# Kernel tuning notes

Measured on AMD Instinct MI355X. Metric: run time of the kernel, lower is better.

## Reference

```python
import jax, jax.numpy as jnp
import numpy as np

B, L, H, N, NL = 32, 512, 768, 64, 4
GAIN = 1.0


def layer_norm(x, w, b, eps=1e-5):
    mu = jnp.mean(x, axis=-1, keepdims=True)
    var = jnp.mean((x - mu) ** 2, axis=-1, keepdims=True)
    return (x - mu) * jax.lax.rsqrt(var + eps) * w + b


def setup_inputs() -> dict:
    key = jax.random.key(0)
    ks = jax.random.split(key, 10)
    x = jax.random.normal(ks[0], (B, L, H), dtype=jnp.float32)
    mask = jnp.ones((B, L), dtype=jnp.int32)
    # S4D parameters per layer (stacked over NL)
    log_dt = jnp.log(10.0 ** jax.random.uniform(ks[1], (NL, H), minval=-3.0, maxval=-1.0))
    A_re = jnp.zeros((NL, H, N), dtype=jnp.float32)  # real part = -exp(0) = -1
    A_im = jnp.broadcast_to(np.pi * jnp.arange(N, dtype=jnp.float32), (NL, H, N)).copy()
    C_re = jax.random.normal(ks[2], (NL, 2, H, N), dtype=jnp.float32) * 0.5 ** 0.5
    C_im = jax.random.normal(ks[3], (NL, 2, H, N), dtype=jnp.float32) * 0.5 ** 0.5
    D = jax.random.normal(ks[4], (NL, H), dtype=jnp.float32)
    Wout = jax.random.normal(ks[5], (NL, H, H), dtype=jnp.float32) / np.sqrt(H)
    bout = jnp.zeros((NL, H), dtype=jnp.float32)
    ln1_w = jnp.ones((NL, H), dtype=jnp.float32)
    ln1_b = jnp.zeros((NL, H), dtype=jnp.float32)
    ln2_w = jnp.ones((NL, H), dtype=jnp.float32)
    ln2_b = jnp.zeros((NL, H), dtype=jnp.float32)
    return dict(x=x, mask=mask, ln1_w=ln1_w, ln1_b=ln1_b, log_dt=log_dt,
                A_re=A_re, A_im=A_im, C_re=C_re, C_im=C_im, D=D,
                Wout=Wout, bout=bout, ln2_w=ln2_w, ln2_b=ln2_b)


def bis4(u, mask_f, log_dt, A_re, A_im, C_re, C_im, D, Wout, bout):
    # u: [B, L, H] (post ln_1); mask_f: [B, L] float
    u = (u * mask_f[:, :, None]).transpose(0, 2, 1)  # [B, H, L]
    dt = jnp.exp(log_dt)  # [H]
    A = (-jnp.exp(A_re) + 1j * A_im).astype(jnp.complex64)  # [H, N]
    dtA = dt[:, None] * A  # [H, N]
    C = (C_re + 1j * C_im).astype(jnp.complex64)  # [2, H, N]
    # ZOH-style: K[d,h,l] = 2 Re sum_n C (e^{dtA}-1)/A * e^{dtA l}
    Cw = C * ((jnp.exp(dtA) - 1.0) / A)  # [2, H, N]
    V = jnp.exp(dtA[:, :, None] * jnp.arange(L, dtype=jnp.float32))  # [H, N, L]
    K = 2.0 * jnp.real(jnp.einsum('dhn,hnl->dhl', Cw, V))  # [2, H, L]
    # bidirectional kernel over circular length 2L
    k_full = (jnp.pad(K[0], ((0, 0), (0, L))) +
              jnp.pad(K[1, :, ::-1], ((0, 0), (L, 0))))  # [H, 2L]
    kf = jnp.fft.rfft(k_full, n=2 * L)           # [H, L+1]
    uf = jnp.fft.rfft(u, n=2 * L)                # [B, H, L+1]
    y = jnp.fft.irfft(uf * kf, n=2 * L)[..., :L]  # [B, H, L]
    y = y + D[:, None] * u
    y = jax.nn.gelu(y)
    y = y.transpose(0, 2, 1)  # [B, L, H]
    return jnp.einsum('blh,oh->blo', y, Wout) + bout


def reference(x, mask, ln1_w, ln1_b, log_dt, A_re, A_im, C_re, C_im, D, Wout, bout, ln2_w, ln2_b):
    mask_f = mask.astype(x.dtype)
    for i in range(NL):
        y = layer_norm(x, ln1_w[i], ln1_b[i])
        y = bis4(y, mask_f, log_dt[i], A_re[i], A_im[i], C_re[i], C_im[i], D[i], Wout[i], bout[i])
        y = layer_norm(y, ln2_w[i], ln2_b[i])
        x = x + y * GAIN
    return x
```

## Files before the change

### kernel.cpp

```cpp
#include <hip/hip_runtime.h>
#include <math.h>

#define BB 32
#define LL 512
#define HH 768
#define NN 64
#define NLAYERS 4

typedef unsigned short ushort;
typedef __attribute__((ext_vector_type(8))) short bf16x8;
typedef __attribute__((ext_vector_type(4))) float f32x4;
typedef __attribute__((ext_vector_type(4))) ushort u16x4;

static __device__ __forceinline__ ushort f2bf(float f) {
  union { float f; unsigned u; } v; v.f = f;
  unsigned r = (v.u + 0x7FFF + ((v.u >> 16) & 1)) >> 16;
  return (ushort)r;
}
static __device__ __forceinline__ float bf2f(ushort u) {
  union { unsigned u; float f; } v; v.u = ((unsigned)u) << 16; return v.f;
}
static __device__ __forceinline__ void gload16(const void* g, void* l) {
  __builtin_amdgcn_global_load_lds(
      (const __attribute__((address_space(1))) unsigned int*)g,
      (__attribute__((address_space(3))) unsigned int*)l, 16, 0, 0);
}
static __device__ __forceinline__ float hw_sin(float f) {
#if __has_builtin(__builtin_amdgcn_sinf)
  return __builtin_amdgcn_sinf(f);
#else
  float r; asm("v_sin_f32 %0, %1" : "=v"(r) : "v"(f)); return r;
#endif
}
static __device__ __forceinline__ float hw_cos(float f) {
#if __has_builtin(__builtin_amdgcn_cosf)
  return __builtin_amdgcn_cosf(f);
#else
  float r; asm("v_cos_f32 %0, %1" : "=v"(r) : "v"(f)); return r;
#endif
}

__global__ __launch_bounds__(256) void compute_k_kernel(
    const float* __restrict__ log_dt, const float* __restrict__ A_re,
    const float* __restrict__ A_im, const float* __restrict__ C_re,
    const float* __restrict__ C_im, ushort* __restrict__ rev) {
  __shared__ float4 cons[4][64][5];
  int wid = threadIdx.x >> 6, lane = threadIdx.x & 63;
  int blk = blockIdx.x * 4 + wid;
  int il = blk / HH, h = blk - il * HH;
  {
    int n = lane;
    float dt = expf(log_dt[blk]);
    float a_re = -expf(A_re[(size_t)blk * NN + n]);
    float a_im = A_im[(size_t)blk * NN + n];
    float er = dt * a_re, ei = dt * a_im;
    float ea = __builtin_amdgcn_exp2f(er * 1.4426950408889634f);
    float fr = ei * 0.15915494309189535f;
    fr = fr - floorf(fr);
    float sv = hw_sin(fr), cv = hw_cos(fr);
    float qr = ea * cv, qi = ea * sv;
    float e1r = qr - 1.f, e1i = qi;
    float den = a_re * a_re + a_im * a_im;
    float wr = (e1r * a_re + e1i * a_im) / den;
    float wi = (e1i * a_re - e1r * a_im) / den;
    size_t c0 = ((size_t)(il * 2 + 0) * HH + h) * NN + n;
    size_t c1 = ((size_t)(il * 2 + 1) * HH + h) * NN + n;
    float c0r = C_re[c0], c0i = C_im[c0];
    float c1r = C_re[c1], c1i = C_im[c1];
    float c0wr = 2.f * (c0r * wr - c0i * wi), c0wi = 2.f * (c0r * wi + c0i * wr);
    float c1wr = 2.f * (c1r * wr - c1i * wi), c1wi = 2.f * (c1r * wi + c1i * wr);
    float pr = qr, pi = qi;
    float P[6][2];
#pragma unroll
    for (int j = 0; j < 8; ++j) {
      float nr = pr * pr - pi * pi, ni = 2.f * pr * pi;
      pr = nr; pi = ni;
      if (j >= 2) { P[j - 2][0] = pr; P[j - 2][1] = pi; }
    }
    cons[wid][n][0] = make_float4(qr, qi, c0wr, c0wi);
    cons[wid][n][1] = make_float4(c1wr, c1wi, P[0][0], P[0][1]);
    cons[wid][n][2] = make_float4(P[1][0], P[1][1], P[2][0], P[2][1]);
    cons[wid][n][3] = make_float4(P[3][0], P[3][1], P[4][0], P[4][1]);
    cons[wid][n][4] = make_float4(P[5][0], P[5][1], 0.f, 0.f);
  }
  __syncthreads();
  int t = lane;
  float k0[8], k1[8];
#pragma unroll
  for (int s = 0; s < 8; ++s) { k0[s] = 0.f; k1[s] = 0.f; }
  for (int n = 0; n < NN; ++n) {
    float4 A0 = cons[wid][n][0];
    float4 A1 = cons[wid][n][1];
    float4 A2 = cons[wid][n][2];
    float4 A3 = cons[wid][n][3];
    float4 A4 = cons[wid][n][4];
    float vr = 1.f, vi = 0.f;
#define MULIF(BIT, PR, PI) { bool c = (t & (BIT)) != 0;                       \
    float nr = vr * (PR) - vi * (PI), ni = vr * (PI) + vi * (PR);             \
    vr = c ? nr : vr; vi = c ? ni : vi; }
    MULIF(1,  A1.z, A1.w)
    MULIF(2,  A2.x, A2.y)
    MULIF(4,  A2.z, A2.w)
    MULIF(8,  A3.x, A3.y)
    MULIF(16, A3.z, A3.w)
    MULIF(32, A4.x, A4.y)
#undef MULIF
#pragma unroll
    for (int s = 0; s < 8; ++s) {
      k0[s] = fmaf(A0.z, vr, fmaf(-A0.w, vi, k0[s]));
      k1[s] = fmaf(A1.x, vr, fmaf(-A1.y, vi, k1[s]));
      float nr = vr * A0.x - vi * A0.y;
      float ni = vr * A0.y + vi * A0.x;
      vr = nr; vi = ni;
    }
  }
  ushort* row = rev + ((size_t)blk << 10);
  bf16x8 o0, o1;
#pragma unroll
  for (int i = 0; i < 8; ++i) {
    o0[i] = (short)f2bf(k0[7 - i]);
    o1[i] = (short)f2bf(k1[i]);
  }
  *(bf16x8*)(row + 504 - 8 * t) = o0;
  *(bf16x8*)(row + 512 + 8 * t) = o1;
}

__global__ __launch_bounds__(256) void wcast_kernel(
    const float* __restrict__ W, ushort* __restrict__ Wbf) {
  size_t i = ((size_t)blockIdx.x * 256 + threadIdx.x) * 8;
  float4 a = *(const float4*)&W[i];
  float4 c = *(const float4*)&W[i + 4];
  ushort o[8] = {f2bf(a.x), f2bf(a.y), f2bf(a.z), f2bf(a.w),
                 f2bf(c.x), f2bf(c.y), f2bf(c.z), f2bf(c.w)};
  *(bf16x8*)&Wbf[i] = *(bf16x8*)o;
}

__global__ __launch_bounds__(256) void ln_t_kernel(
    const float* __restrict__ X, const float* __restrict__ w,
    const float* __restrict__ b, const int* __restrict__ mask,
    ushort* __restrict__ U) {
  __shared__ ushort tile[32][772];
  int bb = blockIdx.y;
  int l0 = blockIdx.x << 5;
  int wv = threadIdx.x >> 6, lane = threadIdx.x & 63;
  const float4* w4 = (const float4*)w;
  const float4* b4 = (const float4*)b;
  float4 WW[3], BV[3];
#pragma unroll
  for (int m = 0; m < 3; ++m) { WW[m] = w4[lane + 64 * m]; BV[m] = b4[lane + 64 * m]; }
#pragma unroll
  for (int i = 0; i < 8; ++i) {
    int r = (wv << 3) + i;
    size_t rowi = (size_t)bb * LL + l0 + r;
    const float4* xr = (const float4*)(X + rowi * HH);
    float4 v[3];
    float s = 0.f, s2 = 0.f;
#pragma unroll
    for (int m = 0; m < 3; ++m) {
      v[m] = xr[lane + 64 * m];
      s  += v[m].x + v[m].y + v[m].z + v[m].w;
      s2 += v[m].x * v[m].x + v[m].y * v[m].y + v[m].z * v[m].z + v[m].w * v[m].w;
    }
#pragma unroll
    for (int off = 32; off >= 1; off >>= 1) {
      s  += __shfl_xor(s, off);
      s2 += __shfl_xor(s2, off);
    }
    float mu  = s * (1.f / HH);
    float var = s2 * (1.f / HH) - mu * mu;
    float rs  = rsqrtf(var + 1e-5f);
    float mf  = (float)mask[rowi];
#pragma unroll
    for (int m = 0; m < 3; ++m) {
      u16x4 o;
      o.x = f2bf(((v[m].x - mu) * rs * WW[m].x + BV[m].x) * mf);
      o.y = f2bf(((v[m].y - mu) * rs * WW[m].y + BV[m].y) * mf);
      o.z = f2bf(((v[m].z - mu) * rs * WW[m].z + BV[m].z) * mf);
      o.w = f2bf(((v[m].w - mu) * rs * WW[m].w + BV[m].w) * mf);
      *(u16x4*)&tile[r][(lane + 64 * m) << 2] = o;
    }
  }
  __syncthreads();
#pragma unroll
  for (int it = 0; it < 3; ++it) {
    int h = it * 256 + threadIdx.x;
    ushort* dst = U + (((size_t)bb * HH + h) << 9) + l0;
#pragma unroll
    for (int c = 0; c < 4; ++c) {
      bf16x8 o;
#pragma unroll
      for (int j = 0; j < 8; ++j) o[j] = (short)tile[c * 8 + j][h];
      *(bf16x8*)(dst + (c << 3)) = o;
    }
  }
}

__global__ __launch_bounds__(256) void ln_res_kernel(
    const float* __restrict__ G, const float* __restrict__ w,
    const float* __restrict__ b, const float* __restrict__ base,
    float* __restrict__ out) {
  int wv = threadIdx.x >> 6, lane = threadIdx.x & 63;
  size_t r = (size_t)blockIdx.x * 4 + wv;
  const float4* gr = (const float4*)(G + r * HH);
  float4 v[3];
  float s = 0.f, s2 = 0.f;
#pragma unroll
  for (int m = 0; m < 3; ++m) {
    v[m] = gr[lane + 64 * m];
    s  += v[m].x + v[m].y + v[m].z + v[m].w;
    s2 += v[m].x * v[m].x + v[m].y * v[m].y + v[m].z * v[m].z + v[m].w * v[m].w;
  }
#pragma unroll
  for (int off = 32; off >= 1; off >>= 1) {
    s  += __shfl_xor(s, off);
    s2 += __shfl_xor(s2, off);
  }
  float mu  = s * (1.f / HH);
  float var = s2 * (1.f / HH) - mu * mu;
  float rs  = rsqrtf(var + 1e-5f);
  const float4* w4 = (const float4*)w;
  const float4* b4 = (const float4*)b;
  const float4* br = (const float4*)(base + r * HH);
  float4* xr = (float4*)(out + r * HH);
#pragma unroll
  for (int m = 0; m < 3; ++m) {
    float4 ww = w4[lane + 64 * m], bb = b4[lane + 64 * m];
    float4 xv = br[lane + 64 * m];
    xv.x += (v[m].x - mu) * rs * ww.x + bb.x;
    xv.y += (v[m].y - mu) * rs * ww.y + bb.y;
    xv.z += (v[m].z - mu) * rs * ww.z + bb.z;
    xv.w += (v[m].w - mu) * rs * ww.w + bb.w;
    xr[lane + 64 * m] = xv;
  }
}

__global__ __launch_bounds__(256) void conv_mfma_kernel(
    const ushort* __restrict__ Ubf, const ushort* __restrict__ rev,
    const float* __restrict__ Dv, ushort* __restrict__ Cbf) {
  __shared__ ushort Ulds[32 * 512];
  __shared__ ushort Ktab[8 * 1048];
  int tid = threadIdx.x;
  int w = tid >> 6, lane = tid & 63;
  int h = blockIdx.x;

#pragma unroll
  for (int it = 0; it < 8; ++it) {
    int G = it * 256 + tid;
    int b = G >> 6, cg = G & 63;
    gload16(Ubf + (((size_t)b * HH + h) << 9) + ((cg ^ (b & 7)) << 3),
            (char*)Ulds + (size_t)(it * 256 + (tid & 0xFFC0)) * 16);
  }
  const ushort* revh = rev + ((size_t)h << 10);
#pragma unroll
  for (int it = 0; it < 5; ++it) {
    int G = it * 256 + tid;
    if (G < 1048) {
      int r = G / 131, pg = G - r * 131;
      int se = (pg << 3) - 17 - r;
      se = se < 0 ? 0 : (se > 1016 ? 1016 : se);
      gload16(revh + se, (char*)Ktab + (size_t)(it * 256 + (tid & 0xFFC0)) * 16);
    }
  }
  asm volatile("s_waitcnt vmcnt(0)" ::: "memory");
  __syncthreads();

  int cc = lane & 15, g = lane >> 4;
  int wt = w << 7;
  const char* kbase = (const char*)Ktab + (cc & 7) * 2096 - ((cc >> 3) << 4)
                      + (g << 4) + 2 * (528 - wt);
  const char* ubase = (const char*)Ulds;
  int usw = (cc & 7) << 4;

  f32x4 acc[8][2];
#pragma unroll
  for (int m = 0; m < 8; ++m)
#pragma unroll
    for (int n = 0; n < 2; ++n) acc[m][n] = (f32x4){0.f, 0.f, 0.f, 0.f};

  bf16x8 A[8];
#define LDA(slot, m, ks) A[slot] = *(const bf16x8*)(kbase - (m) * 32 + (ks) * 64)
  LDA(0, 0, 0); LDA(1, 1, 0); LDA(2, 2, 0); LDA(3, 3, 0);
  LDA(4, 4, 0); LDA(5, 5, 0); LDA(6, 6, 0); LDA(7, 7, 0);
#pragma unroll
  for (int ks = 0; ks < 16; ++ks) {
    if (ks > 0) {
      LDA((0 - 2 * ks) & 7, 0, ks);
      LDA((1 - 2 * ks) & 7, 1, ks);
    }
    int ub = ((ks << 6) + (g << 4)) ^ usw;
    bf16x8 B0 = *(const bf16x8*)(ubase + cc * 1024 + ub);
    bf16x8 B1 = *(const bf16x8*)(ubase + (16 + cc) * 1024 + ub);
#pragma unroll
    for (int m = 0; m < 8; ++m) {
      acc[m][0] = __builtin_amdgcn_mfma_f32_16x16x32_bf16(
          A[(m - 2 * ks) & 7], B0, acc[m][0], 0, 0, 0);
      acc[m][1] = __builtin_amdgcn_mfma_f32_16x16x32_bf16(
          A[(m - 2 * ks) & 7], B1, acc[m][1], 0, 0, 0);
    }
  }
#undef LDA

  float dh = Dv[h];
  const float c1 = 2.3021181306612f, c3 = 0.1029392186f;
#pragma unroll
  for (int n = 0; n < 2; ++n) {
    int b = (n << 4) + cc;
    const char* up = (const char*)Ulds + b * 1024;
#pragma unroll
    for (int m = 0; m < 8; ++m) {
      int t0 = wt + (m << 4) + (g << 2);
      u16x4 uq = *(const u16x4*)(up + ((t0 << 1) ^ usw));
      u16x4 o;
#pragma unroll
      for (int r = 0; r < 4; ++r) {
        float y = acc[m][n][r] + dh * bf2f(uq[r]);
        float e = __builtin_amdgcn_exp2f(-(c1 * y + c3 * y * y * y));
        float gg = y * __builtin_amdgcn_rcpf(1.f + e);
        o[r] = f2bf(gg);
      }
      *(u16x4*)(Cbf + (((size_t)b * HH + h) << 9) + t0) = o;
    }
  }
}

__global__ __launch_bounds__(256) void t2bf_bf_kernel(
    const ushort* __restrict__ C, ushort* __restrict__ Y) {
  __shared__ ushort tile[32][34];
  int b = blockIdx.z;
  int h0 = blockIdx.x << 5, l0 = blockIdx.y << 5;
  int tx = threadIdx.x, ty = threadIdx.y;
#pragma unroll
  for (int k = 0; k < 4; ++k)
    tile[ty + 8 * k][tx] = C[(((size_t)b * HH + h0 + ty + 8 * k) << 9) + l0 + tx];
  __syncthreads();
#pragma unroll
  for (int k = 0; k < 4; ++k)
    Y[((size_t)b * LL + l0 + ty + 8 * k) * HH + h0 + tx] = tile[tx][ty + 8 * k];
}

__global__ __launch_bounds__(256) void gemm_kernel(
    const ushort* __restrict__ Ybf, const ushort* __restrict__ Wbf,
    const float* __restrict__ bias, float* __restrict__ G) {
  __shared__ ushort As[128 * 64];
  __shared__ ushort Bs[128 * 64];
  int tid = threadIdx.x;
  int wv = tid >> 6, lane = tid & 63;
  int wm = wv >> 1, wn = wv & 1;
  int b  = blockIdx.y >> 2;
  int l0 = (blockIdx.y & 3) << 7;
  int o0 = blockIdx.x << 7;

  int swz8 = (((lane & 7) ^ (lane >> 3)) << 3);
  int rsub = (lane >> 3);
  size_t arow0 = (size_t)(b * LL + l0 + wv * 32 + rsub) * HH;
  size_t brow0 = (size_t)(o0 + wv * 32 + rsub) * HH;
  char* Adst = (char*)As + wv * 4096;
  char* Bdst = (char*)Bs + wv * 4096;

  f32x4 acc[4][4];
#pragma unroll
  for (int i = 0; i < 4; ++i)
#pragma unroll
    for (int j = 0; j < 4; ++j) acc[i][j] = (f32x4){0.f, 0.f, 0.f, 0.f};

  for (int kt = 0; kt < HH / 64; ++kt) {
    int h0 = kt * 64;
#pragma unroll
    for (int i = 0; i < 4; ++i) {
      gload16(Ybf + arow0 + (size_t)i * 8 * HH + h0 + swz8, Adst + i * 1024);
      gload16(Wbf + brow0 + (size_t)i * 8 * HH + h0 + swz8, Bdst + i * 1024);
    }
    __syncthreads();

    bf16x8 af[4][2], bfr[4][2];
#pragma unroll
    for (int mi = 0; mi < 4; ++mi) {
      int m = wm * 64 + mi * 16 + (lane & 15);
#pragma unroll
      for (int kk = 0; kk < 2; ++kk) {
        int off = m * 128 + ((((lane >> 4) << 4) + (kk << 6)) ^ ((lane & 7) << 4));
        af[mi][kk] = *(const bf16x8*)((const char*)As + off);
      }
    }
#pragma unroll
    for (int ni = 0; ni < 4; ++ni) {
      int n = wn * 64 + ni * 16 + (lane & 15);
#pragma unroll
      for (int kk = 0; kk < 2; ++kk) {
        int off = n * 128 + ((((lane >> 4) << 4) + (kk << 6)) ^ ((lane & 7) << 4));
        bfr[ni][kk] = *(const bf16x8*)((const char*)Bs + off);
      }
    }
#pragma unroll
    for (int kk = 0; kk < 2; ++kk)
#pragma unroll
      for (int mi = 0; mi < 4; ++mi)
#pragma unroll
        for (int ni = 0; ni < 4; ++ni)
          acc[mi][ni] = __builtin_amdgcn_mfma_f32_16x16x32_bf16(
              af[mi][kk], bfr[ni][kk], acc[mi][ni], 0, 0, 0);
    __syncthreads();
  }

#pragma unroll
  for (int ni = 0; ni < 4; ++ni) {
    int n_g = o0 + wn * 64 + ni * 16 + (lane & 15);
    float bv = bias[n_g];
#pragma unroll
    for (int mi = 0; mi < 4; ++mi) {
      int m_g = l0 + wm * 64 + mi * 16 + ((lane >> 4) << 2);
      float* gp = G + ((size_t)b * LL + m_g) * HH + n_g;
#pragma unroll
      for (int j = 0; j < 4; ++j)
        gp[(size_t)j * HH] = acc[mi][ni][j] + bv;
    }
  }
}

extern "C" void kernel_launch(void* const* d_in, const int* in_sizes, int n_in,
                              void* d_out, int out_size, void* d_ws, size_t ws_size,
                              hipStream_t stream) {
  const float* x      = (const float*)d_in[0];
  const int*   mask   = (const int*)d_in[1];
  const float* ln1_w  = (const float*)d_in[2];
  const float* ln1_b  = (const float*)d_in[3];
  const float* log_dt = (const float*)d_in[4];
  const float* A_re   = (const float*)d_in[5];
  const float* A_im   = (const float*)d_in[6];
  const float* C_re   = (const float*)d_in[7];
  const float* C_im   = (const float*)d_in[8];
  const float* Dv     = (const float*)d_in[9];
  const float* Wout   = (const float*)d_in[10];
  const float* bout   = (const float*)d_in[11];
  const float* ln2_w  = (const float*)d_in[12];
  const float* ln2_b  = (const float*)d_in[13];
  float* out = (float*)d_out;

  ushort* rev  = (ushort*)d_ws;
  ushort* Ubf  = rev + (size_t)NLAYERS * HH * 1024;
  ushort* Cbf  = Ubf + (size_t)BB * HH * LL;
  ushort* Wbf  = Cbf + (size_t)BB * HH * LL;
  float*  Gf   = (float*)(Wbf + (size_t)NLAYERS * HH * HH);
  ushort* Ybf  = Ubf;

  compute_k_kernel<<<NLAYERS * HH / 4, 256, 0, stream>>>(
      log_dt, A_re, A_im, C_re, C_im, rev);
  wcast_kernel<<<(NLAYERS * HH * HH) / (256 * 8), 256, 0, stream>>>(Wout, Wbf);

  for (int il = 0; il < NLAYERS; ++il) {
    const float* src = (il == 0) ? x : out;
    ln_t_kernel<<<dim3(LL / 32, BB), 256, 0, stream>>>(
        src, ln1_w + il * HH, ln1_b + il * HH, mask, Ubf);
    conv_mfma_kernel<<<HH, 256, 0, stream>>>(
        Ubf, rev + (size_t)il * HH * 1024, Dv + il * HH, Cbf);
    t2bf_bf_kernel<<<dim3(HH / 32, LL / 32, BB), dim3(32, 8), 0, stream>>>(Cbf, Ybf);
    gemm_kernel<<<dim3(HH / 128, BB * LL / 128), 256, 0, stream>>>(
        Ybf, Wbf + (size_t)il * HH * HH, bout + il * HH, Gf);
    ln_res_kernel<<<BB * LL / 4, 256, 0, stream>>>(
        Gf, ln2_w + il * HH, ln2_b + il * HH, src, out);
  }
}
```

Baseline: 564.1 us.

## Fuse residual LN with next-layer LN/transpose, store GEMM output as bf16

Adds a res_lnt kernel that applies LN2 and the residual update, then the next layer's LN1, mask and transpose in a single pass. This removes a separate read of the residual stream per layer. The GEMM now writes its output in bf16 instead of fp32, halving that intermediate's traffic at the cost of extra rounding before LN2. compute_k is also reorganised so two waves split the N dimension per channel and reduce through LDS, which raises parallelism for that kernel.

```diff
diff --git a/kernel.cpp b/kernel.cpp
--- a/kernel.cpp
+++ b/kernel.cpp
@@ -26,30 +26,24 @@
       (__attribute__((address_space(3))) unsigned int*)l, 16, 0, 0);
 }
 static __device__ __forceinline__ float hw_sin(float f) {
-#if __has_builtin(__builtin_amdgcn_sinf)
-  return __builtin_amdgcn_sinf(f);
-#else
   float r; asm("v_sin_f32 %0, %1" : "=v"(r) : "v"(f)); return r;
-#endif
 }
 static __device__ __forceinline__ float hw_cos(float f) {
-#if __has_builtin(__builtin_amdgcn_cosf)
-  return __builtin_amdgcn_cosf(f);
-#else
   float r; asm("v_cos_f32 %0, %1" : "=v"(r) : "v"(f)); return r;
-#endif
 }
 
 __global__ __launch_bounds__(256) void compute_k_kernel(
     const float* __restrict__ log_dt, const float* __restrict__ A_re,
     const float* __restrict__ A_im, const float* __restrict__ C_re,
     const float* __restrict__ C_im, ushort* __restrict__ rev) {
-  __shared__ float4 cons[4][64][5];
+  __shared__ float4 cons[2][64][5];
+  __shared__ float red[2][64][17];
   int wid = threadIdx.x >> 6, lane = threadIdx.x & 63;
-  int blk = blockIdx.x * 4 + wid;
+  int p = wid >> 1, nh = wid & 1;
+  int blk = blockIdx.x * 2 + p;
   int il = blk / HH, h = blk - il * HH;
-  {
-    int n = lane;
+  if (lane < 32) {
+    int n = nh * 32 + lane;
     float dt = expf(log_dt[blk]);
     float a_re = -expf(A_re[(size_t)blk * NN + n]);
     float a_im = A_im[(size_t)blk * NN + n];
@@ -77,23 +71,24 @@
       pr = nr; pi = ni;
       if (j >= 2) { P[j - 2][0] = pr; P[j - 2][1] = pi; }
     }
-    cons[wid][n][0] = make_float4(qr, qi, c0wr, c0wi);
-    cons[wid][n][1] = make_float4(c1wr, c1wi, P[0][0], P[0][1]);
-    cons[wid][n][2] = make_float4(P[1][0], P[1][1], P[2][0], P[2][1]);
-    cons[wid][n][3] = make_float4(P[3][0], P[3][1], P[4][0], P[4][1]);
-    cons[wid][n][4] = make_float4(P[5][0], P[5][1], 0.f, 0.f);
+    cons[p][n][0] = make_float4(qr, qi, c0wr, c0wi);
+    cons[p][n][1] = make_float4(c1wr, c1wi, P[0][0], P[0][1]);
+    cons[p][n][2] = make_float4(P[1][0], P[1][1], P[2][0], P[2][1]);
+    cons[p][n][3] = make_float4(P[3][0], P[3][1], P[4][0], P[4][1]);
+    cons[p][n][4] = make_float4(P[5][0], P[5][1], 0.f, 0.f);
   }
   __syncthreads();
   int t = lane;
   float k0[8], k1[8];
 #pragma unroll
   for (int s = 0; s < 8; ++s) { k0[s] = 0.f; k1[s] = 0.f; }
-  for (int n = 0; n < NN; ++n) {
-    float4 A0 = cons[wid][n][0];
-    float4 A1 = cons[wid][n][1];
-    float4 A2 = cons[wid][n][2];
-    float4 A3 = cons[wid][n][3];
-    float4 A4 = cons[wid][n][4];
+  for (int nn = 0; nn < 32; ++nn) {
+    int n = nh * 32 + nn;
+    float4 A0 = cons[p][n][0];
+    float4 A1 = cons[p][n][1];
+    float4 A2 = cons[p][n][2];
+    float4 A3 = cons[p][n][3];
+    float4 A4 = cons[p][n][4];
     float vr = 1.f, vi = 0.f;
 #define MULIF(BIT, PR, PI) { bool c = (t & (BIT)) != 0;                       \
     float nr = vr * (PR) - vi * (PI), ni = vr * (PI) + vi * (PR);             \
@@ -114,15 +109,30 @@
       vr = nr; vi = ni;
     }
   }
-  ushort* row = rev + ((size_t)blk << 10);
-  bf16x8 o0, o1;
-#pragma unroll
-  for (int i = 0; i < 8; ++i) {
-    o0[i] = (short)f2bf(k0[7 - i]);
-    o1[i] = (short)f2bf(k1[i]);
-  }
-  *(bf16x8*)(row + 504 - 8 * t) = o0;
-  *(bf16x8*)(row + 512 + 8 * t) = o1;
+  if (nh == 1) {
+#pragma unroll
+    for (int s = 0; s < 8; ++s) {
+      red[p][lane][s] = k0[s];
+      red[p][lane][8 + s] = k1[s];
+    }
+  }
+  __syncthreads();
+  if (nh == 0) {
+#pragma unroll
+    for (int s = 0; s < 8; ++s) {
+      k0[s] += red[p][lane][s];
+      k1[s] += red[p][lane][8 + s];
+    }
+    ushort* row = rev + ((size_t)blk << 10);
+    bf16x8 o0, o1;
+#pragma unroll
+    for (int i = 0; i < 8; ++i) {
+      o0[i] = (short)f2bf(k0[7 - i]);
+      o1[i] = (short)f2bf(k1[i]);
+    }
+    *(bf16x8*)(row + 504 - 8 * t) = o0;
+    *(bf16x8*)(row + 512 + 8 * t) = o1;
+  }
 }
 
 __global__ __launch_bounds__(256) void wcast_kernel(
@@ -195,20 +205,121 @@
   }
 }
 
+__global__ __launch_bounds__(256) void res_lnt_kernel(
+    const ushort* __restrict__ Gbf, const float* __restrict__ w2,
+    const float* __restrict__ b2, const float* __restrict__ base,
+    float* __restrict__ out, const int* __restrict__ mask,
+    const float* __restrict__ w1, const float* __restrict__ b1,
+    ushort* __restrict__ U) {
+  __shared__ ushort tile[32][772];
+  int bb = blockIdx.y;
+  int l0 = blockIdx.x << 5;
+  int wv = threadIdx.x >> 6, lane = threadIdx.x & 63;
+  const float4* w14 = (const float4*)w1;
+  const float4* b14 = (const float4*)b1;
+  const float4* w24 = (const float4*)w2;
+  const float4* b24 = (const float4*)b2;
+  float4 W1[3], B1[3], W2[3], B2[3];
+#pragma unroll
+  for (int m = 0; m < 3; ++m) {
+    W1[m] = w14[lane + 64 * m]; B1[m] = b14[lane + 64 * m];
+    W2[m] = w24[lane + 64 * m]; B2[m] = b24[lane + 64 * m];
+  }
+#pragma unroll
+  for (int i = 0; i < 8; ++i) {
+    int r = (wv << 3) + i;
+    size_t rowi = (size_t)bb * LL + l0 + r;
+    const u16x4* gr = (const u16x4*)(Gbf + rowi * HH);
+    float gv[12];
+    float s = 0.f, s2 = 0.f;
+#pragma unroll
+    for (int m = 0; m < 3; ++m) {
+      u16x4 q = gr[lane + 64 * m];
+#pragma unroll
+      for (int j = 0; j < 4; ++j) {
+        float f = bf2f(q[j]);
+        gv[m * 4 + j] = f;
+        s += f; s2 += f * f;
+      }
+    }
+#pragma unroll
+    for (int off = 32; off >= 1; off >>= 1) {
+      s  += __shfl_xor(s, off);
+      s2 += __shfl_xor(s2, off);
+    }
+    float mu2  = s * (1.f / HH);
+    float var2 = s2 * (1.f / HH) - mu2 * mu2;
+    float rs2  = rsqrtf(var2 + 1e-5f);
+    const float4* br = (const float4*)(base + rowi * HH);
+    float4* orow = (float4*)(out + rowi * HH);
+    float ov[12];
+    float t1 = 0.f, t2 = 0.f;
+#pragma unroll
+    for (int m = 0; m < 3; ++m) {
+      float4 bv = br[lane + 64 * m];
+      float4 o;
+      o.x = bv.x + (gv[m * 4 + 0] - mu2) * rs2 * W2[m].x + B2[m].x;
+      o.y = bv.y + (gv[m * 4 + 1] - mu2) * rs2 * W2[m].y + B2[m].y;
+      o.z = bv.z + (gv[m * 4 + 2] - mu2) * rs2 * W2[m].z + B2[m].z;
+      o.w = bv.w + (gv[m * 4 + 3] - mu2) * rs2 * W2[m].w + B2[m].w;
+      orow[lane + 64 * m] = o;
+      ov[m * 4 + 0] = o.x; ov[m * 4 + 1] = o.y;
+      ov[m * 4 + 2] = o.z; ov[m * 4 + 3] = o.w;
+      t1 += o.x + o.y + o.z + o.w;
+      t2 += o.x * o.x + o.y * o.y + o.z * o.z + o.w * o.w;
+    }
+#pragma unroll
+    for (int off = 32; off >= 1; off >>= 1) {
+      t1 += __shfl_xor(t1, off);
+      t2 += __shfl_xor(t2, off);
+    }
+    float mu1  = t1 * (1.f / HH);
+    float var1 = t2 * (1.f / HH) - mu1 * mu1;
+    float rs1  = rsqrtf(var1 + 1e-5f);
+    float mf   = (float)mask[rowi];
+#pragma unroll
+    for (int m = 0; m < 3; ++m) {
+      u16x4 o;
+      o.x = f2bf(((ov[m * 4 + 0] - mu1) * rs1 * W1[m].x + B1[m].x) * mf);
+      o.y = f2bf(((ov[m * 4 + 1] - mu1) * rs1 * W1[m].y + B1[m].y) * mf);
+      o.z = f2bf(((ov[m * 4 + 2] - mu1) * rs1 * W1[m].z + B1[m].z) * mf);
+      o.w = f2bf(((ov[m * 4 + 3] - mu1) * rs1 * W1[m].w + B1[m].w) * mf);
+      *(u16x4*)&tile[r][(lane + 64 * m) << 2] = o;
+    }
+  }
+  __syncthreads();
+#pragma unroll
+  for (int it = 0; it < 3; ++it) {
+    int h = it * 256 + threadIdx.x;
+    ushort* dst = U + (((size_t)bb * HH + h) << 9) + l0;
+#pragma unroll
+    for (int c = 0; c < 4; ++c) {
+      bf16x8 o;
+#pragma unroll
+      for (int j = 0; j < 8; ++j) o[j] = (short)tile[c * 8 + j][h];
+      *(bf16x8*)(dst + (c << 3)) = o;
+    }
+  }
+}
+
 __global__ __launch_bounds__(256) void ln_res_kernel(
-    const float* __restrict__ G, const float* __restrict__ w,
+    const ushort* __restrict__ Gbf, const float* __restrict__ w,
     const float* __restrict__ b, const float* __restrict__ base,
     float* __restrict__ out) {
   int wv = threadIdx.x >> 6, lane = threadIdx.x & 63;
   size_t r = (size_t)blockIdx.x * 4 + wv;
-  const float4* gr = (const float4*)(G + r * HH);
-  float4 v[3];
+  const u16x4* gr = (const u16x4*)(Gbf + r * HH);
+  float gv[12];
   float s = 0.f, s2 = 0.f;
 #pragma unroll
   for (int m = 0; m < 3; ++m) {
-    v[m] = gr[lane + 64 * m];
-    s  += v[m].x + v[m].y + v[m].z + v[m].w;
-    s2 += v[m].x * v[m].x + v[m].y * v[m].y + v[m].z * v[m].z + v[m].w * v[m].w;
+    u16x4 q = gr[lane + 64 * m];
+#pragma unroll
+    for (int j = 0; j < 4; ++j) {
+      float f = bf2f(q[j]);
+      gv[m * 4 + j] = f;
+      s += f; s2 += f * f;
+    }
   }
 #pragma unroll
   for (int off = 32; off >= 1; off >>= 1) {
@@ -226,10 +337,10 @@
   for (int m = 0; m < 3; ++m) {
     float4 ww = w4[lane + 64 * m], bb = b4[lane + 64 * m];
     float4 xv = br[lane + 64 * m];
-    xv.x += (v[m].x - mu) * rs * ww.x + bb.x;
-    xv.y += (v[m].y - mu) * rs * ww.y + bb.y;
-    xv.z += (v[m].z - mu) * rs * ww.z + bb.z;
-    xv.w += (v[m].w - mu) * rs * ww.w + bb.w;
+    xv.x += (gv[m * 4 + 0] - mu) * rs * ww.x + bb.x;
+    xv.y += (gv[m * 4 + 1] - mu) * rs * ww.y + bb.y;
+    xv.z += (gv[m * 4 + 2] - mu) * rs * ww.z + bb.z;
+    xv.w += (gv[m * 4 + 3] - mu) * rs * ww.w + bb.w;
     xr[lane + 64 * m] = xv;
   }
 }
@@ -340,7 +451,7 @@
 
 __global__ __launch_bounds__(256) void gemm_kernel(
     const ushort* __restrict__ Ybf, const ushort* __restrict__ Wbf,
-    const float* __restrict__ bias, float* __restrict__ G) {
+    const float* __restrict__ bias, ushort* __restrict__ Gb) {
   __shared__ ushort As[128 * 64];
   __shared__ ushort Bs[128 * 64];
   int tid = threadIdx.x;
@@ -409,10 +520,10 @@
 #pragma unroll
     for (int mi = 0; mi < 4; ++mi) {
       int m_g = l0 + wm * 64 + mi * 16 + ((lane >> 4) << 2);
-      float* gp = G + ((size_t)b * LL + m_g) * HH + n_g;
+      ushort* gp = Gb + ((size_t)b * LL + m_g) * HH + n_g;
 #pragma unroll
       for (int j = 0; j < 4; ++j)
-        gp[(size_t)j * HH] = acc[mi][ni][j] + bv;
+        gp[(size_t)j * HH] = f2bf(acc[mi][ni][j] + bv);
     }
   }
 }
@@ -440,23 +551,30 @@
   ushort* Ubf  = rev + (size_t)NLAYERS * HH * 1024;
   ushort* Cbf  = Ubf + (size_t)BB * HH * LL;
   ushort* Wbf  = Cbf + (size_t)BB * HH * LL;
-  float*  Gf   = (float*)(Wbf + (size_t)NLAYERS * HH * HH);
+  ushort* Gbf  = Wbf + (size_t)NLAYERS * HH * HH;
   ushort* Ybf  = Ubf;
 
-  compute_k_kernel<<<NLAYERS * HH / 4, 256, 0, stream>>>(
+  compute_k_kernel<<<NLAYERS * HH / 2, 256, 0, stream>>>(
       log_dt, A_re, A_im, C_re, C_im, rev);
   wcast_kernel<<<(NLAYERS * HH * HH) / (256 * 8), 256, 0, stream>>>(Wout, Wbf);
 
+  ln_t_kernel<<<dim3(LL / 32, BB), 256, 0, stream>>>(
+      x, ln1_w, ln1_b, mask, Ubf);
+
   for (int il = 0; il < NLAYERS; ++il) {
-    const float* src = (il == 0) ? x : out;
-    ln_t_kernel<<<dim3(LL / 32, BB), 256, 0, stream>>>(
-        src, ln1_w + il * HH, ln1_b + il * HH, mask, Ubf);
+    const float* base = (il == 0) ? x : out;
     conv_mfma_kernel<<<HH, 256, 0, stream>>>(
         Ubf, rev + (size_t)il * HH * 1024, Dv + il * HH, Cbf);
     t2bf_bf_kernel<<<dim3(HH / 32, LL / 32, BB), dim3(32, 8), 0, stream>>>(Cbf, Ybf);
     gemm_kernel<<<dim3(HH / 128, BB * LL / 128), 256, 0, stream>>>(
-        Ybf, Wbf + (size_t)il * HH * HH, bout + il * HH, Gf);
-    ln_res_kernel<<<BB * LL / 4, 256, 0, stream>>>(
-        Gf, ln2_w + il * HH, ln2_b + il * HH, src, out);
-  }
-}
+        Ybf, Wbf + (size_t)il * HH * HH, bout + il * HH, Gbf);
+    if (il < NLAYERS - 1) {
+      res_lnt_kernel<<<dim3(LL / 32, BB), 256, 0, stream>>>(
+          Gbf, ln2_w + il * HH, ln2_b + il * HH, base, out,
+          mask, ln1_w + (il + 1) * HH, ln1_b + (il + 1) * HH, Ubf);
+    } else {
+      ln_res_kernel<<<BB * LL / 4, 256, 0, stream>>>(
+          Gbf, ln2_w + il * HH, ln2_b + il * HH, base, out);
+    }
+  }
+}
```

Result: faster. 526.6 us (-6.6%).
